# Kernel tuning notes

Hardware: AMD Instinct MI355X
Metric: run time of the kernel (lower is better)

The kernel has to match this reference:

```python
import jax, jax.numpy as jnp
import numpy as np

N, E, F_IN, H, D = 50000, 800000, 128, 4, 32


def setup_inputs() -> dict:
    key = jax.random.key(0)
    k_x, k_e, k_w, k_al, k_ar = jax.random.split(key, 5)
    x = jax.random.normal(k_x, (N, F_IN), dtype=jnp.float32)
    edge_index = jax.random.randint(k_e, (2, E), 0, N, dtype=jnp.int32).astype(jnp.int64)
    # xavier-uniform-like scales
    s_w = float(np.sqrt(6.0 / (F_IN + H * D)))
    s_a = float(np.sqrt(6.0 / (D + 1)))
    W = jax.random.uniform(k_w, (F_IN, H * D), jnp.float32, -s_w, s_w)
    att_l = jax.random.uniform(k_al, (H, D), jnp.float32, -s_a, s_a)
    att_r = jax.random.uniform(k_ar, (H, D), jnp.float32, -s_a, s_a)
    bias = jnp.zeros((H * D,), jnp.float32)
    return {"x": x, "edge_index": edge_index, "W": W, "att_l": att_l, "att_r": att_r, "bias": bias}


def reference(x, edge_index, W, att_l, att_r, bias):
    num_nodes = x.shape[0]
    n_heads, head_dim = att_l.shape
    h = (x @ W).reshape(num_nodes, n_heads, head_dim)          # [N,H,D]
    alpha_l = jnp.einsum('nhd,hd->nh', h, att_l)               # [N,H]
    alpha_r = jnp.einsum('nhd,hd->nh', h, att_r)               # [N,H]
    from_idx, to_idx = edge_index[0], edge_index[1]
    att = alpha_l[from_idx] + alpha_r[to_idx]                  # [E,H]
    att = jax.nn.leaky_relu(att, negative_slope=0.2)
    # segment softmax over edges grouped by destination node (shift by global
    # per-head max, exactly as the source's _softmax effectively does)
    att = att - jax.lax.stop_gradient(jnp.max(att, axis=0, keepdims=True))
    ex = jnp.exp(att)                                          # [E,H]
    denom = jax.ops.segment_sum(ex, to_idx, num_segments=num_nodes)  # [N,H]
    att_n = ex / (denom[to_idx] + 1e-9)                        # [E,H]
    # scatter-weighted aggregation: out[n] = sum_{e: to=n} att[e] * h[from[e]]
    msgs = att_n[:, :, None] * h[from_idx]                     # [E,H,D]
    out = jax.ops.segment_sum(msgs, to_idx, num_segments=num_nodes)  # [N,H,D]
    out = out.reshape(num_nodes, n_heads * head_dim) + bias
    return out
```

## Files before the change

### kernel.cpp

```cpp
#include <hip/hip_runtime.h>
#include <cstdint>

#define N_NODES 50000
#define N_EDGES 800000
#define F_IN    128
#define N_HEADS 4
#define HEAD_DIM 32
#define F_OUT   128

#define NBUCK   391
#define NPB     128
#define KA_GRID 512
#define EPB     1563
#define EPB_PAD 1568
#define REC_CAP 2560
#define STAGE_CAP REC_CAP
#define NSTRIP  (N_NODES / 16)
#define NGEMM   ((NSTRIP + 3) / 4)

typedef unsigned int uint32;
typedef unsigned short ushort;
typedef __attribute__((ext_vector_type(8))) short short8v;
typedef __attribute__((ext_vector_type(4))) float float4v;

typedef __attribute__((address_space(1))) const ushort gushort;
typedef __attribute__((address_space(3))) ushort lushort;

__device__ __forceinline__ ushort f2bf(float f) {
    uint32 u = __float_as_uint(f);
    return (ushort)((u + 0x7FFFu + ((u >> 16) & 1u)) >> 16);
}


__device__ __forceinline__ int block_scan_excl_256(int v, int* p_total)
{
    const int t = threadIdx.x, lane = t & 63, wv = t >> 6;
    int incl = v;
#pragma unroll
    for (int d = 1; d < 64; d <<= 1) {
        int u = __shfl_up(incl, d);
        if (lane >= d) incl += u;
    }
    __shared__ int wsum[4];
    if (lane == 63) wsum[wv] = incl;
    __syncthreads();
    int woff = 0;
#pragma unroll
    for (int j = 0; j < 4; ++j) {
        int s = wsum[j];
        if (j < wv) woff += s;
    }
    if (p_total) *p_total = wsum[0] + wsum[1] + wsum[2] + wsum[3];
    __syncthreads();
    return woff + incl - v;
}

__global__ __launch_bounds__(256) void k_prep(const float* __restrict__ W,
    ushort* __restrict__ WTF)
{
    const int id = blockIdx.x * 256 + threadIdx.x;
    if (id >= 32 * 64) return;
    const int tile = id >> 6, l = id & 63;
    const int q = l >> 4, c15 = l & 15;
    const int nt = tile >> 2, kt = tile & 3;
    short8v hv, lv;
#pragma unroll
    for (int j = 0; j < 8; ++j) {
        const int k = kt * 32 + q * 8 + j;
        const float w = W[k * F_OUT + nt * 16 + c15];
        const ushort hi = f2bf(w);
        const float hif = __uint_as_float((uint32)hi << 16);
        hv[j] = (short)hi;
        lv[j] = (short)f2bf(w - hif);
    }
    *(short8v*)&WTF[tile * 512 + l * 8]         = hv;
    *(short8v*)&WTF[16384 + tile * 512 + l * 8] = lv;
}

__global__ __launch_bounds__(256, 2) void k_bin_gemm(
    const int* __restrict__ ei, const float* __restrict__ x,
    const ushort* __restrict__ WTF,
    const float* __restrict__ attl, const float* __restrict__ attr,
    uint32* __restrict__ blockarr, int* __restrict__ cnts, int* __restrict__ offs,
    uint32* __restrict__ hbq, float* __restrict__ aLp, float* __restrict__ aRp)
{
    __shared__ __attribute__((aligned(16))) char lds_buf[65536];

    if (blockIdx.x < KA_GRID) {
        int*    cur = (int*)lds_buf;
        int*    off = cur + 512;
        uint32* stg = (uint32*)(off + 512);
        const int sb = blockIdx.x, t = threadIdx.x;

        cur[t] = 0; cur[t + 256] = 0;
        __syncthreads();

        const int e0 = sb * EPB;
        const int lim = min(EPB, N_EDGES - e0);
        for (int i = t; i < lim; i += 256)
            atomicAdd(&cur[ei[N_EDGES + e0 + i] >> 7], 1);
        __syncthreads();

        const int c0 = cur[2 * t], c1 = cur[2 * t + 1];
        const int ex = block_scan_excl_256(c0 + c1, nullptr);
        off[2 * t]     = ex;
        off[2 * t + 1] = ex + c0;
        __syncthreads();

        for (int bb = t; bb < NBUCK; bb += 256) {
            cnts[(size_t)bb * KA_GRID + sb] = cur[bb];
            offs[(size_t)bb * KA_GRID + sb] = off[bb];
        }
        __syncthreads();

        for (int i = t; i < lim; i += 256) {
            const int from = ei[e0 + i];
            const int to   = ei[N_EDGES + e0 + i];
            const int pos = atomicAdd(&off[to >> 7], 1);
            stg[pos] = (uint32)from | ((uint32)(to & 127) << 16);
        }
        __syncthreads();

        uint32* dst = blockarr + (size_t)sb * EPB_PAD;
        for (int i = t; i < lim; i += 256)
            dst[i] = stg[i];
        return;
    }

    const int bid   = blockIdx.x - KA_GRID;
    const int lane  = threadIdx.x & 63;
    const int wv    = threadIdx.x >> 6;
    const int q     = lane >> 4;
    const int c15   = lane & 15;

    ushort* wt = (ushort*)lds_buf;
#pragma unroll
    for (int i = 0; i < 16; ++i) {
        const int chunk = wv * 16 + i;
        __builtin_amdgcn_global_load_lds(
            (gushort*)(WTF + chunk * 512 + lane * 8),
            (lushort*)(wt + chunk * 512), 16, 0, 0);
    }
    __syncthreads();

    const int strip = bid * 4 + wv;
    if (strip >= NSTRIP) return;
    const int row0 = strip * 16;

    const float* xrow = x + (size_t)(row0 + c15) * F_IN + q * 8;
    short8v ahi[4], alo[4];
#pragma unroll
    for (int kt = 0; kt < 4; ++kt) {
        const float4 f0 = *(const float4*)(xrow + kt * 32);
        const float4 f1 = *(const float4*)(xrow + kt * 32 + 4);
        const float fs[8] = {f0.x, f0.y, f0.z, f0.w, f1.x, f1.y, f1.z, f1.w};
#pragma unroll
        for (int j = 0; j < 8; ++j) {
            const ushort hi = f2bf(fs[j]);
            const float hif = __uint_as_float((uint32)hi << 16);
            ahi[kt][j] = (short)hi;
            alo[kt][j] = (short)f2bf(fs[j] - hif);
        }
    }

    float4v acc[8];
#pragma unroll
    for (int nt = 0; nt < 8; ++nt) {
        float4v a = {0.f, 0.f, 0.f, 0.f};
#pragma unroll
        for (int kt = 0; kt < 4; ++kt) {
            const short8v bh = *(const short8v*)(wt + (nt * 4 + kt) * 512 + lane * 8);
            const short8v bl = *(const short8v*)(wt + 16384 + (nt * 4 + kt) * 512 + lane * 8);
            a = __builtin_amdgcn_mfma_f32_16x16x32_bf16(ahi[kt], bh, a, 0, 0, 0);
            a = __builtin_amdgcn_mfma_f32_16x16x32_bf16(alo[kt], bh, a, 0, 0, 0);
            a = __builtin_amdgcn_mfma_f32_16x16x32_bf16(ahi[kt], bl, a, 0, 0, 0);
        }
        acc[nt] = a;
    }

#pragma unroll
    for (int nt = 0; nt < 4; ++nt) {
#pragma unroll
        for (int r = 0; r < 4; ++r) {
            const uint32 d = (uint32)f2bf(acc[nt][r]) | ((uint32)f2bf(acc[nt + 4][r]) << 16);
            hbq[(size_t)(row0 + q * 4 + r) * 64 + nt * 16 + c15] = d;
        }
    }

    float aLacc[4][4] = {{0.f}}, aRacc[4][4] = {{0.f}};
#pragma unroll
    for (int nt = 0; nt < 8; ++nt) {
        const float alv = attl[nt * 16 + c15];
        const float arv = attr[nt * 16 + c15];
        const int hh = nt >> 1;
#pragma unroll
        for (int r = 0; r < 4; ++r) {
            aLacc[r][hh] = fmaf(acc[nt][r], alv, aLacc[r][hh]);
            aRacc[r][hh] = fmaf(acc[nt][r], arv, aRacc[r][hh]);
        }
    }
#pragma unroll
    for (int r = 0; r < 4; ++r) {
#pragma unroll
        for (int hh = 0; hh < 4; ++hh) {
            float vl = aLacc[r][hh], vr = aRacc[r][hh];
#pragma unroll
            for (int d = 1; d < 16; d <<= 1) {
                vl += __shfl_xor(vl, d);
                vr += __shfl_xor(vr, d);
            }
            if (c15 == hh) {
                const int row = row0 + q * 4 + r;
                const int pos = (hh & 1) * 2 + (hh >> 1);
                aLp[row * N_HEADS + pos] = vl;
                aRp[row * N_HEADS + pos] = vr;
            }
        }
    }
}

__global__ __launch_bounds__(256) void k_build(const uint32* __restrict__ blockarr,
    const int* __restrict__ cnts, const int* __restrict__ offs,
    const float* __restrict__ aLp, const float* __restrict__ aRp,
    int* __restrict__ count, int* __restrict__ offsets, int* __restrict__ rec_from,
    float* __restrict__ wexp)
{
    __shared__ uint32 stage[STAGE_CAP];
    __shared__ int hist[NPB], curn[NPB];
    __shared__ float aR[NPB * 4];
    const int b = blockIdx.x, t = threadIdx.x;

    if (t < NPB) {
        const int nn = b * NPB + t;
        float4 v = make_float4(0.f, 0.f, 0.f, 0.f);
        if (nn < N_NODES) v = *(const float4*)&aRp[(size_t)nn * 4];
        *(float4*)&aR[t * 4] = v;
    }

    int c[2], o[2];
#pragma unroll
    for (int j = 0; j < 2; ++j) {
        c[j] = cnts[(size_t)b * KA_GRID + 2 * t + j];
        o[j] = offs[(size_t)b * KA_GRID + 2 * t + j];
    }
    int total;
    int ex = block_scan_excl_256(c[0] + c[1], &total);
    if (t < NPB) hist[t] = 0;
    __syncthreads();

#pragma unroll
    for (int j = 0; j < 2; ++j) {
        const int sb = 2 * t + j;
        const uint32* src = blockarr + (size_t)sb * EPB_PAD + o[j];
        for (int i = 0; i < c[j]; ++i) {
            const int p = ex + i;
            if (p < STAGE_CAP) stage[p] = src[i];
        }
        ex += c[j];
    }
    __syncthreads();

    const int S = min(total, STAGE_CAP);
    for (int i = t; i < S; i += 256) atomicAdd(&hist[stage[i] >> 16], 1);
    __syncthreads();

    const int hv = (t < NPB) ? hist[t] : 0;
    int tot2;
    const int lo = block_scan_excl_256(hv, &tot2);
    const int rbase = b * REC_CAP;
    const int n = b * NPB + t;
    if (t < NPB && n < N_NODES) {
        count[n]   = hv;
        offsets[n] = rbase + lo;
    }
    if (t < NPB) curn[t] = lo;
    __syncthreads();

    for (int i = t; i < S; i += 256) {
        const uint32 e = stage[i];
        const int toloc = e >> 16;
        const int from  = (int)(e & 0xFFFFu);
        const int pos = atomicAdd(&curn[toloc], 1);
        const float4 al = *(const float4*)&aLp[(size_t)from * 4];
        const float4 ar = *(const float4*)&aR[toloc * 4];
        float t0 = al.x + ar.x; t0 = (t0 > 0.f) ? t0 : 0.2f * t0;
        float t1 = al.y + ar.y; t1 = (t1 > 0.f) ? t1 : 0.2f * t1;
        float t2 = al.z + ar.z; t2 = (t2 > 0.f) ? t2 : 0.2f * t2;
        float t3 = al.w + ar.w; t3 = (t3 > 0.f) ? t3 : 0.2f * t3;
        rec_from[rbase + pos] = from;
        *(float4*)&wexp[(size_t)(rbase + pos) * 4] =
            make_float4(__expf(t0), __expf(t1), __expf(t2), __expf(t3));
    }
}

__global__ __launch_bounds__(256) void k_agg(const int* __restrict__ rec_from,
    const int* __restrict__ count, const int* __restrict__ offsets,
    const float* __restrict__ wexp, const uint32* __restrict__ hbq,
    const float* __restrict__ bias, float* __restrict__ out)
{
    const int lane = threadIdx.x & 63;
    const int n = blockIdx.x * 4 + (threadIdx.x >> 6);
    if (n >= N_NODES) return;
    const int cnt = __builtin_amdgcn_readfirstlane(count[n]);
    const int off = __builtin_amdgcn_readfirstlane(offsets[n]);
    const int hsel = (lane >> 5) * 2;
    const int epair = hsel >> 1;
    const float2* wex2 = (const float2*)wexp;

    float ax = 0.f, ay = 0.f, ds0 = 0.f, ds1 = 0.f;
    int i = 0;
    for (; i + 8 <= cnt; i += 8) {
        int f[8]; uint32 h[8]; float2 e[8];
#pragma unroll
        for (int j = 0; j < 8; ++j) f[j] = rec_from[off + i + j];
#pragma unroll
        for (int j = 0; j < 8; ++j) h[j] = hbq[(size_t)f[j] * 64 + lane];
#pragma unroll
        for (int j = 0; j < 8; ++j) e[j] = wex2[(size_t)(off + i + j) * 2 + epair];
#pragma unroll
        for (int j = 0; j < 8; ++j) {
            ax = fmaf(e[j].x, __uint_as_float(h[j] << 16), ax);
            ay = fmaf(e[j].y, __uint_as_float(h[j] & 0xFFFF0000u), ay);
            ds0 += e[j].x; ds1 += e[j].y;
        }
    }
    for (; i + 4 <= cnt; i += 4) {
        int f[4]; uint32 h[4]; float2 e[4];
#pragma unroll
        for (int j = 0; j < 4; ++j) f[j] = rec_from[off + i + j];
#pragma unroll
        for (int j = 0; j < 4; ++j) h[j] = hbq[(size_t)f[j] * 64 + lane];
#pragma unroll
        for (int j = 0; j < 4; ++j) e[j] = wex2[(size_t)(off + i + j) * 2 + epair];
#pragma unroll
        for (int j = 0; j < 4; ++j) {
            ax = fmaf(e[j].x, __uint_as_float(h[j] << 16), ax);
            ay = fmaf(e[j].y, __uint_as_float(h[j] & 0xFFFF0000u), ay);
            ds0 += e[j].x; ds1 += e[j].y;
        }
    }
    for (; i < cnt; ++i) {
        const int f = rec_from[off + i];
        const uint32 hv = hbq[(size_t)f * 64 + lane];
        const float2 e = wex2[(size_t)(off + i) * 2 + epair];
        ax = fmaf(e.x, __uint_as_float(hv << 16), ax);
        ay = fmaf(e.y, __uint_as_float(hv & 0xFFFF0000u), ay);
        ds0 += e.x; ds1 += e.y;
    }

    const float inv0 = 1.0f / (ds0 + 1e-9f);
    const float inv1 = 1.0f / (ds1 + 1e-9f);
    out[n * F_OUT + lane]      = ax * inv0 + bias[lane];
    out[n * F_OUT + 64 + lane] = ay * inv1 + bias[64 + lane];
}

extern "C" void kernel_launch(void* const* d_in, const int* in_sizes, int n_in,
                              void* d_out, int out_size, void* d_ws, size_t ws_size,
                              hipStream_t stream)
{
    const float* x    = (const float*)d_in[0];
    const int*   ei   = (const int*)d_in[1];
    const float* W    = (const float*)d_in[2];
    const float* attl = (const float*)d_in[3];
    const float* attr = (const float*)d_in[4];
    const float* bias = (const float*)d_in[5];
    float* out = (float*)d_out;

    char* p = (char*)d_ws;
    auto carve = [&](size_t bytes) -> char* {
        char* q = p;
        p += (bytes + 255) & ~size_t(255);
        return q;
    };
    uint32* hbq      = (uint32*)carve((size_t)N_NODES * 64 * 4);
    uint32* blockarr = (uint32*)carve((size_t)KA_GRID * EPB_PAD * 4);
    int*    rec_from = (int*)carve((size_t)NBUCK * REC_CAP * 4);
    float*  wexp     = (float*)carve((size_t)NBUCK * REC_CAP * 4 * 4);
    ushort* WTF      = (ushort*)carve(32768 * 2);
    float*  aLp      = (float*)carve((size_t)N_NODES * N_HEADS * 4);
    float*  aRp      = (float*)carve((size_t)N_NODES * N_HEADS * 4);
    int*    cnts     = (int*)carve((size_t)NBUCK * KA_GRID * 4);
    int*    offs     = (int*)carve((size_t)NBUCK * KA_GRID * 4);
    int*    count    = (int*)carve((size_t)N_NODES * 4);
    int*    offsets  = (int*)carve((size_t)N_NODES * 4);

    k_prep<<<8, 256, 0, stream>>>(W, WTF);
    k_bin_gemm<<<KA_GRID + NGEMM, 256, 0, stream>>>(ei, x, WTF,
                                                    attl, attr, blockarr,
                                                    cnts, offs,
                                                    hbq, aLp, aRp);
    k_build<<<NBUCK, 256, 0, stream>>>(blockarr, cnts, offs, aLp, aRp,
                                       count, offsets, rec_from, wexp);
    k_agg<<<(N_NODES + 3) / 4, 256, 0, stream>>>(rec_from, count, offsets,
                                                 wexp, hbq, bias, out);
}
```

Before: 161.6 us.

## Fuse CSR build and aggregation into one kernel with LDS-resident edge lists

Merges the per-bucket build kernel and the aggregation kernel into one. Each block now owns 64 destination nodes instead of 128, keeps the sorted source list in shared memory, and recomputes leaky-relu and exp per edge from aLp rather than writing and re-reading rec_from and wexp arrays through global memory. This removes one launch and the global round-trip of per-edge records. In exchange, exp work is repeated per lane pair, only 782 blocks of 4 waves do the gather (less parallelism per node set), and the smaller stage capacity risks truncation when a bucket's edge count exceeds 1408.

```diff
diff --git a/kernel.cpp b/kernel.cpp
--- a/kernel.cpp
+++ b/kernel.cpp
@@ -8,13 +8,12 @@
 #define HEAD_DIM 32
 #define F_OUT   128
 
-#define NBUCK   391
-#define NPB     128
+#define NBUCK   782
+#define NPB     64
 #define KA_GRID 512
 #define EPB     1563
 #define EPB_PAD 1568
-#define REC_CAP 2560
-#define STAGE_CAP REC_CAP
+#define STAGE_CAP 1408
 #define NSTRIP  (N_NODES / 16)
 #define NGEMM   ((NSTRIP + 3) / 4)
 
@@ -88,23 +87,26 @@
 
     if (blockIdx.x < KA_GRID) {
         int*    cur = (int*)lds_buf;
-        int*    off = cur + 512;
-        uint32* stg = (uint32*)(off + 512);
+        int*    off = cur + 1024;
+        uint32* stg = (uint32*)(off + 1024);
         const int sb = blockIdx.x, t = threadIdx.x;
 
-        cur[t] = 0; cur[t + 256] = 0;
+        cur[t] = 0; cur[t + 256] = 0; cur[t + 512] = 0; cur[t + 768] = 0;
         __syncthreads();
 
         const int e0 = sb * EPB;
         const int lim = min(EPB, N_EDGES - e0);
         for (int i = t; i < lim; i += 256)
-            atomicAdd(&cur[ei[N_EDGES + e0 + i] >> 7], 1);
-        __syncthreads();
-
-        const int c0 = cur[2 * t], c1 = cur[2 * t + 1];
-        const int ex = block_scan_excl_256(c0 + c1, nullptr);
-        off[2 * t]     = ex;
-        off[2 * t + 1] = ex + c0;
+            atomicAdd(&cur[ei[N_EDGES + e0 + i] >> 6], 1);
+        __syncthreads();
+
+        const int c0 = cur[4 * t], c1 = cur[4 * t + 1];
+        const int c2 = cur[4 * t + 2], c3 = cur[4 * t + 3];
+        const int ex = block_scan_excl_256(c0 + c1 + c2 + c3, nullptr);
+        off[4 * t]     = ex;
+        off[4 * t + 1] = ex + c0;
+        off[4 * t + 2] = ex + c0 + c1;
+        off[4 * t + 3] = ex + c0 + c1 + c2;
         __syncthreads();
 
         for (int bb = t; bb < NBUCK; bb += 256) {
@@ -116,8 +118,8 @@
         for (int i = t; i < lim; i += 256) {
             const int from = ei[e0 + i];
             const int to   = ei[N_EDGES + e0 + i];
-            const int pos = atomicAdd(&off[to >> 7], 1);
-            stg[pos] = (uint32)from | ((uint32)(to & 127) << 16);
+            const int pos = atomicAdd(&off[to >> 6], 1);
+            stg[pos] = (uint32)from | ((uint32)(to & 63) << 16);
         }
         __syncthreads();
 
@@ -219,14 +221,15 @@
     }
 }
 
-__global__ __launch_bounds__(256) void k_build(const uint32* __restrict__ blockarr,
+__global__ __launch_bounds__(256) void k_build_agg(const uint32* __restrict__ blockarr,
     const int* __restrict__ cnts, const int* __restrict__ offs,
     const float* __restrict__ aLp, const float* __restrict__ aRp,
-    int* __restrict__ count, int* __restrict__ offsets, int* __restrict__ rec_from,
-    float* __restrict__ wexp)
+    const uint32* __restrict__ hbq,
+    const float* __restrict__ bias, float* __restrict__ out)
 {
     __shared__ uint32 stage[STAGE_CAP];
-    __shared__ int hist[NPB], curn[NPB];
+    __shared__ uint32 rec[STAGE_CAP];
+    __shared__ int hist[NPB], curn[NPB], off_l[NPB], cnt_l[NPB];
     __shared__ float aR[NPB * 4];
     const int b = blockIdx.x, t = threadIdx.x;
 
@@ -235,6 +238,7 @@
         float4 v = make_float4(0.f, 0.f, 0.f, 0.f);
         if (nn < N_NODES) v = *(const float4*)&aRp[(size_t)nn * 4];
         *(float4*)&aR[t * 4] = v;
+        hist[t] = 0;
     }
 
     int c[2], o[2];
@@ -245,7 +249,6 @@
     }
     int total;
     int ex = block_scan_excl_256(c[0] + c[1], &total);
-    if (t < NPB) hist[t] = 0;
     __syncthreads();
 
 #pragma unroll
@@ -267,91 +270,70 @@
     const int hv = (t < NPB) ? hist[t] : 0;
     int tot2;
     const int lo = block_scan_excl_256(hv, &tot2);
-    const int rbase = b * REC_CAP;
-    const int n = b * NPB + t;
-    if (t < NPB && n < N_NODES) {
-        count[n]   = hv;
-        offsets[n] = rbase + lo;
-    }
-    if (t < NPB) curn[t] = lo;
+    if (t < NPB) {
+        off_l[t] = lo;
+        cnt_l[t] = hv;
+        curn[t]  = lo;
+    }
     __syncthreads();
 
     for (int i = t; i < S; i += 256) {
         const uint32 e = stage[i];
-        const int toloc = e >> 16;
-        const int from  = (int)(e & 0xFFFFu);
-        const int pos = atomicAdd(&curn[toloc], 1);
-        const float4 al = *(const float4*)&aLp[(size_t)from * 4];
-        const float4 ar = *(const float4*)&aR[toloc * 4];
-        float t0 = al.x + ar.x; t0 = (t0 > 0.f) ? t0 : 0.2f * t0;
-        float t1 = al.y + ar.y; t1 = (t1 > 0.f) ? t1 : 0.2f * t1;
-        float t2 = al.z + ar.z; t2 = (t2 > 0.f) ? t2 : 0.2f * t2;
-        float t3 = al.w + ar.w; t3 = (t3 > 0.f) ? t3 : 0.2f * t3;
-        rec_from[rbase + pos] = from;
-        *(float4*)&wexp[(size_t)(rbase + pos) * 4] =
-            make_float4(__expf(t0), __expf(t1), __expf(t2), __expf(t3));
-    }
-}
-
-__global__ __launch_bounds__(256) void k_agg(const int* __restrict__ rec_from,
-    const int* __restrict__ count, const int* __restrict__ offsets,
-    const float* __restrict__ wexp, const uint32* __restrict__ hbq,
-    const float* __restrict__ bias, float* __restrict__ out)
-{
-    const int lane = threadIdx.x & 63;
-    const int n = blockIdx.x * 4 + (threadIdx.x >> 6);
-    if (n >= N_NODES) return;
-    const int cnt = __builtin_amdgcn_readfirstlane(count[n]);
-    const int off = __builtin_amdgcn_readfirstlane(offsets[n]);
+        const int pos = atomicAdd(&curn[e >> 16], 1);
+        rec[pos] = e & 0xFFFFu;
+    }
+    __syncthreads();
+
+    const int lane = t & 63;
+    const int wv   = t >> 6;
     const int hsel = (lane >> 5) * 2;
     const int epair = hsel >> 1;
-    const float2* wex2 = (const float2*)wexp;
-
-    float ax = 0.f, ay = 0.f, ds0 = 0.f, ds1 = 0.f;
-    int i = 0;
-    for (; i + 8 <= cnt; i += 8) {
-        int f[8]; uint32 h[8]; float2 e[8];
-#pragma unroll
-        for (int j = 0; j < 8; ++j) f[j] = rec_from[off + i + j];
-#pragma unroll
-        for (int j = 0; j < 8; ++j) h[j] = hbq[(size_t)f[j] * 64 + lane];
-#pragma unroll
-        for (int j = 0; j < 8; ++j) e[j] = wex2[(size_t)(off + i + j) * 2 + epair];
-#pragma unroll
-        for (int j = 0; j < 8; ++j) {
-            ax = fmaf(e[j].x, __uint_as_float(h[j] << 16), ax);
-            ay = fmaf(e[j].y, __uint_as_float(h[j] & 0xFFFF0000u), ay);
-            ds0 += e[j].x; ds1 += e[j].y;
-        }
-    }
-    for (; i + 4 <= cnt; i += 4) {
-        int f[4]; uint32 h[4]; float2 e[4];
-#pragma unroll
-        for (int j = 0; j < 4; ++j) f[j] = rec_from[off + i + j];
-#pragma unroll
-        for (int j = 0; j < 4; ++j) h[j] = hbq[(size_t)f[j] * 64 + lane];
-#pragma unroll
-        for (int j = 0; j < 4; ++j) e[j] = wex2[(size_t)(off + i + j) * 2 + epair];
-#pragma unroll
-        for (int j = 0; j < 4; ++j) {
-            ax = fmaf(e[j].x, __uint_as_float(h[j] << 16), ax);
-            ay = fmaf(e[j].y, __uint_as_float(h[j] & 0xFFFF0000u), ay);
-            ds0 += e[j].x; ds1 += e[j].y;
-        }
-    }
-    for (; i < cnt; ++i) {
-        const int f = rec_from[off + i];
-        const uint32 hv = hbq[(size_t)f * 64 + lane];
-        const float2 e = wex2[(size_t)(off + i) * 2 + epair];
-        ax = fmaf(e.x, __uint_as_float(hv << 16), ax);
-        ay = fmaf(e.y, __uint_as_float(hv & 0xFFFF0000u), ay);
-        ds0 += e.x; ds1 += e.y;
-    }
-
-    const float inv0 = 1.0f / (ds0 + 1e-9f);
-    const float inv1 = 1.0f / (ds1 + 1e-9f);
-    out[n * F_OUT + lane]      = ax * inv0 + bias[lane];
-    out[n * F_OUT + 64 + lane] = ay * inv1 + bias[64 + lane];
+    const float2* aLp2 = (const float2*)aLp;
+
+    for (int r = wv; r < NPB; r += 4) {
+        const int n = b * NPB + r;
+        if (n >= N_NODES) break;
+        const int cnt = __builtin_amdgcn_readfirstlane(cnt_l[r]);
+        const int off = __builtin_amdgcn_readfirstlane(off_l[r]);
+        const float2 arv = *(const float2*)&aR[r * 4 + hsel];
+
+        float ax = 0.f, ay = 0.f, ds0 = 0.f, ds1 = 0.f;
+        int i = 0;
+        for (; i + 8 <= cnt; i += 8) {
+            int f[8]; uint32 h[8]; float2 al[8];
+#pragma unroll
+            for (int j = 0; j < 8; ++j) f[j] = rec[off + i + j];
+#pragma unroll
+            for (int j = 0; j < 8; ++j) h[j] = hbq[(size_t)f[j] * 64 + lane];
+#pragma unroll
+            for (int j = 0; j < 8; ++j) al[j] = aLp2[(size_t)f[j] * 2 + epair];
+#pragma unroll
+            for (int j = 0; j < 8; ++j) {
+                float t0 = al[j].x + arv.x; t0 = fmaxf(t0, 0.2f * t0);
+                float t1 = al[j].y + arv.y; t1 = fmaxf(t1, 0.2f * t1);
+                const float e0 = __expf(t0), e1 = __expf(t1);
+                ax = fmaf(e0, __uint_as_float(h[j] << 16), ax);
+                ay = fmaf(e1, __uint_as_float(h[j] & 0xFFFF0000u), ay);
+                ds0 += e0; ds1 += e1;
+            }
+        }
+        for (; i < cnt; ++i) {
+            const int f = rec[off + i];
+            const uint32 hv2 = hbq[(size_t)f * 64 + lane];
+            const float2 al = aLp2[(size_t)f * 2 + epair];
+            float t0 = al.x + arv.x; t0 = fmaxf(t0, 0.2f * t0);
+            float t1 = al.y + arv.y; t1 = fmaxf(t1, 0.2f * t1);
+            const float e0 = __expf(t0), e1 = __expf(t1);
+            ax = fmaf(e0, __uint_as_float(hv2 << 16), ax);
+            ay = fmaf(e1, __uint_as_float(hv2 & 0xFFFF0000u), ay);
+            ds0 += e0; ds1 += e1;
+        }
+
+        const float inv0 = 1.0f / (ds0 + 1e-9f);
+        const float inv1 = 1.0f / (ds1 + 1e-9f);
+        out[n * F_OUT + lane]      = ax * inv0 + bias[lane];
+        out[n * F_OUT + 64 + lane] = ay * inv1 + bias[64 + lane];
+    }
 }
 
 extern "C" void kernel_launch(void* const* d_in, const int* in_sizes, int n_in,
@@ -374,23 +356,17 @@
     };
     uint32* hbq      = (uint32*)carve((size_t)N_NODES * 64 * 4);
     uint32* blockarr = (uint32*)carve((size_t)KA_GRID * EPB_PAD * 4);
-    int*    rec_from = (int*)carve((size_t)NBUCK * REC_CAP * 4);
-    float*  wexp     = (float*)carve((size_t)NBUCK * REC_CAP * 4 * 4);
     ushort* WTF      = (ushort*)carve(32768 * 2);
     float*  aLp      = (float*)carve((size_t)N_NODES * N_HEADS * 4);
     float*  aRp      = (float*)carve((size_t)N_NODES * N_HEADS * 4);
     int*    cnts     = (int*)carve((size_t)NBUCK * KA_GRID * 4);
     int*    offs     = (int*)carve((size_t)NBUCK * KA_GRID * 4);
-    int*    count    = (int*)carve((size_t)N_NODES * 4);
-    int*    offsets  = (int*)carve((size_t)N_NODES * 4);
 
     k_prep<<<8, 256, 0, stream>>>(W, WTF);
     k_bin_gemm<<<KA_GRID + NGEMM, 256, 0, stream>>>(ei, x, WTF,
                                                     attl, attr, blockarr,
                                                     cnts, offs,
                                                     hbq, aLp, aRp);
-    k_build<<<NBUCK, 256, 0, stream>>>(blockarr, cnts, offs, aLp, aRp,
-                                       count, offsets, rec_from, wexp);
-    k_agg<<<(N_NODES + 3) / 4, 256, 0, stream>>>(rec_from, count, offsets,
-                                                 wexp, hbq, bias, out);
-}
+    k_build_agg<<<NBUCK, 256, 0, stream>>>(blockarr, cnts, offs,
+                                           aLp, aRp, hbq, bias, out);
+}
```

Measured after the change: 181.7 us. 1.12x slower.
